# Optimization experiments

Measured on AMD Instinct MI355X. Metric: run time of the kernel, lower is better.

Reference implementation:

```python
import jax, jax.numpy as jnp
import numpy as np

SR = 48000
HARMONIC_NUM = 8          # -> 9 harmonics total
SINE_AMP = 0.1
NOISE_STD = 0.003
VOICED_THRESHOLD = 0.0
B, T, UPP = 8, 2000, 480
S = T * UPP


def setup_inputs() -> dict:
    key = jax.random.key(0)
    k_f0, k_mask, k_ri, k_noise = jax.random.split(key, 4)
    f0 = jax.random.uniform(k_f0, (B, 1, T), jnp.float32, 80.0, 500.0)
    voiced = (jax.random.uniform(k_mask, (B, 1, T)) > 0.2).astype(jnp.float32)
    f0 = f0 * voiced
    # random initial phases; harmonic 0 gets phase 0 (as in torch code)
    rand_ini = jax.random.uniform(k_ri, (B, HARMONIC_NUM + 1), jnp.float32)
    rand_ini = rand_ini.at[:, 0].set(0.0)
    noise_raw = jax.random.normal(k_noise, (B, S), jnp.float32)
    # linear mixing layer: weight = 1/(H+1), bias = 0 per nn.init in __init__
    w = jnp.full((HARMONIC_NUM + 1,), 1.0 / (HARMONIC_NUM + 1), jnp.float32)
    b = jnp.zeros((1,), jnp.float32)
    return {"f0": f0, "rand_ini": rand_ini, "noise_raw": noise_raw,
            "w": w, "b": b, "upp": UPP}


def reference(f0, rand_ini, noise_raw, w, b, upp):
    # f0: [B,1,T] Hz -> nearest-upsample to [B, S]
    f0u = jnp.repeat(f0[:, 0, :], upp, axis=1)              # [B, S]
    uv = (f0u > VOICED_THRESHOLD).astype(f0.dtype)          # [B, S]
    rad = f0u * (2.0 * np.pi / SR)
    # cumsum is linear: one cumsum, broadcast-multiply by harmonic index
    base_phase = jnp.cumsum(rad, axis=1)                    # [B, S]
    mult = jnp.arange(1, HARMONIC_NUM + 2, dtype=f0.dtype)  # [H+1]
    phase = base_phase[:, :, None] * mult + rand_ini[:, None, :] * (2.0 * np.pi)
    sines = jnp.sin(phase) * uv[:, :, None]                 # [B, S, H+1]
    har = jnp.tanh(sines @ w + b[0]) * SINE_AMP             # [B, S]
    noise = noise_raw * NOISE_STD                            # [B, S]
    return har[:, None, :], noise[:, None, :], uv[:, None, :]
```

## Files before the change

### kernel.cpp

```cpp
#include <hip/hip_runtime.h>
#include <hip/hip_bf16.h>
#include <math.h>

constexpr int   B_   = 8;
constexpr int   T_   = 2000;
constexpr int   UPP_ = 480;
constexpr int   S_   = T_ * UPP_;
constexpr int   NH   = 9;
constexpr int   SPT  = 4;
constexpr int   BLK  = 320;
constexpr int   QPR  = S_ / SPT;
constexpr int   BPR  = QPR / BLK;
constexpr float INV_SR = 1.0f / 48000.0f;

typedef float fx4 __attribute__((ext_vector_type(4)));

#if __has_builtin(__builtin_amdgcn_sinf)
__device__ __forceinline__ float sinrev(float x) { return __builtin_amdgcn_sinf(x); }
#else
__device__ __forceinline__ float sinrev(float x) { return __sinf(x * 6.2831853071795864769f); }
#endif
#if __has_builtin(__builtin_amdgcn_cosf)
__device__ __forceinline__ float cosrev(float x) { return __builtin_amdgcn_cosf(x); }
#else
__device__ __forceinline__ float cosrev(float x) { return __cosf(x * 6.2831853071795864769f); }
#endif

__device__ __forceinline__ void nt_store4(float* p, float a, float b, float c, float d) {
    fx4 v = {a, b, c, d};
    __builtin_nontemporal_store(v, (fx4*)p);
}
__device__ __forceinline__ fx4 nt_load4(const float* p) {
    return __builtin_nontemporal_load((const fx4*)p);
}

__global__ __launch_bounds__(256) void frame_scan_kernel(
    const float* __restrict__ f0,
    const float* __restrict__ rand_ini,
    const float* __restrict__ w,
    float2* __restrict__ ftab,
    float2* __restrict__ abtab)
{
    __shared__ double wsum[4];
    const int b    = blockIdx.x;
    const int j    = threadIdx.x;
    const int lane = j & 63;
    const int wid  = j >> 6;
    constexpr int CH = 8;
    const int t0 = j * CH;

    if (j < NH) {
        float ri = rand_ini[b * NH + j];
        float wv = w[j];
        abtab[b * NH + j] = make_float2(wv * cosrev(ri), wv * sinrev(ri));
    }

    float fc[CH];
    double local = 0.0;
    #pragma unroll
    for (int k = 0; k < CH; ++k) {
        int t = t0 + k;
        float v = (t < T_) ? f0[b * T_ + t] : 0.0f;
        fc[k] = v * INV_SR;
        local += (double)fc[k] * (double)UPP_;
    }

    double x = local;
    #pragma unroll
    for (int off = 1; off < 64; off <<= 1) {
        double y = __shfl_up(x, off, 64);
        if (lane >= off) x += y;
    }
    if (lane == 63) wsum[wid] = x;
    __syncthreads();

    double woff = 0.0;
    #pragma unroll
    for (int ww = 0; ww < 3; ++ww)
        if (ww < wid) woff += wsum[ww];

    double excl = (x + woff) - local;

    #pragma unroll
    for (int k = 0; k < CH; ++k) {
        int t = t0 + k;
        if (t < T_) {
            double ph = excl - floor(excl);
            ftab[b * T_ + t] = make_float2((float)ph, fc[k]);
            excl += (double)fc[k] * (double)UPP_;
        }
    }
}

__global__ __launch_bounds__(BLK) void synth_kernel(
    const float* __restrict__ noise_raw,
    const float* __restrict__ bb,
    const float2* __restrict__ ftab,
    const float2* __restrict__ abtab,
    float* __restrict__ out)
{
    const int bblk = blockIdx.x / BPR;
    const int rblk = blockIdx.x - bblk * BPR;
    const int q    = rblk * BLK + threadIdx.x;
    const int s0   = q * SPT;
    const int t    = s0 / UPP_;
    const int i0   = s0 - t * UPP_;

    float A[NH], Bc[NH];
    #pragma unroll
    for (int h = 0; h < NH; ++h) {
        float2 ab = abtab[bblk * NH + h];
        A[h]  = ab.x;
        Bc[h] = ab.y;
    }
    const float bias = bb[0];

    const float2 pf   = ftab[bblk * T_ + t];
    const float  Pred = pf.x;
    const float  fcyc = pf.y;
    const float  uvf  = (fcyc > 0.0f) ? 1.0f : 0.0f;

    const size_t row = (size_t)bblk * S_ + s0;
    const fx4 nz = nt_load4(noise_raw + row);

    float har[SPT];
    #pragma unroll
    for (int k = 0; k < SPT; ++k) {
        float base = Pred + fcyc * (float)(i0 + 1 + k);
        float f    = base - floorf(base);
        float s1   = sinrev(f);
        float c1   = cosrev(f);
        float tc   = c1 + c1;
        float sm1 = 0.0f, cm1 = 1.0f;
        float sm  = s1,   cm  = c1;
        float acc = 0.0f;
        #pragma unroll
        for (int h = 0; h < NH; ++h) {
            acc = fmaf(sm, A[h], acc);
            acc = fmaf(cm, Bc[h], acc);
            float sn = fmaf(tc, sm, -sm1);
            float cn = fmaf(tc, cm, -cm1);
            sm1 = sm; cm1 = cm; sm = sn; cm = cn;
        }
        float xx = fmaf(acc, uvf, bias);
        float e  = __expf(2.0f * xx);
        har[k]   = (e - 1.0f) / (e + 1.0f) * 0.1f;
    }

    float* harp = out;
    float* nzp  = out + (size_t)B_ * S_;
    float* uvp  = out + (size_t)2 * B_ * S_;

    nt_store4(harp + row, har[0], har[1], har[2], har[3]);
    nt_store4(nzp + row,  nz.x * 0.003f, nz.y * 0.003f, nz.z * 0.003f, nz.w * 0.003f);
    nt_store4(uvp + row,  uvf, uvf, uvf, uvf);
}

extern "C" void kernel_launch(void* const* d_in, const int* in_sizes, int n_in,
                              void* d_out, int out_size, void* d_ws, size_t ws_size,
                              hipStream_t stream) {
    const float* f0        = (const float*)d_in[0];
    const float* rand_ini  = (const float*)d_in[1];
    const float* noise_raw = (const float*)d_in[2];
    const float* w         = (const float*)d_in[3];
    const float* bb        = (const float*)d_in[4];

    float2* ftab  = (float2*)d_ws;
    float2* abtab = (float2*)((char*)d_ws + 128000);

    frame_scan_kernel<<<B_, 256, 0, stream>>>(f0, rand_ini, w, ftab, abtab);
    synth_kernel<<<B_ * BPR, BLK, 0, stream>>>(
        noise_raw, bb, ftab, abtab, (float*)d_out);
}
```

Measured before the change: 31.14 us.

## Fuse frame prefix scan into synth kernel with per-block redundant reduction

Removes the separate frame-scan kernel and its workspace tables. Each synth block now sums the f0 values of all frames before its start in a block-wide double reduction, and each thread adds the few frames between the block start and its own sample. The phase is then computed inline. This saves one kernel launch and the dependency between the two kernels, at the cost of redundant reads of f0 per block: up to 2000 values per block across 6000 blocks, plus double-precision adds and a __syncthreads.

```diff
diff --git a/kernel.cpp b/kernel.cpp
--- a/kernel.cpp
+++ b/kernel.cpp
@@ -9,9 +9,12 @@
 constexpr int   NH   = 9;
 constexpr int   SPT  = 4;
 constexpr int   BLK  = 320;
+constexpr int   SPB  = BLK * SPT;
 constexpr int   QPR  = S_ / SPT;
 constexpr int   BPR  = QPR / BLK;
+constexpr int   NWAVE = BLK / 64;
 constexpr float INV_SR = 1.0f / 48000.0f;
+constexpr double CYC_PER_F0 = (double)UPP_ / 48000.0;
 
 typedef float fx4 __attribute__((ext_vector_type(4)));
 
@@ -34,91 +37,71 @@
     return __builtin_nontemporal_load((const fx4*)p);
 }
 
-__global__ __launch_bounds__(256) void frame_scan_kernel(
+__global__ __launch_bounds__(BLK) void fused_kernel(
     const float* __restrict__ f0,
     const float* __restrict__ rand_ini,
+    const float* __restrict__ noise_raw,
     const float* __restrict__ w,
-    float2* __restrict__ ftab,
-    float2* __restrict__ abtab)
+    const float* __restrict__ bb,
+    float* __restrict__ out)
 {
-    __shared__ double wsum[4];
-    const int b    = blockIdx.x;
-    const int j    = threadIdx.x;
-    const int lane = j & 63;
-    const int wid  = j >> 6;
-    constexpr int CH = 8;
-    const int t0 = j * CH;
+    __shared__ double wpart[NWAVE];
+    __shared__ float2 ab_s[NH];
 
-    if (j < NH) {
-        float ri = rand_ini[b * NH + j];
-        float wv = w[j];
-        abtab[b * NH + j] = make_float2(wv * cosrev(ri), wv * sinrev(ri));
+    const int bblk = blockIdx.x / BPR;
+    const int rblk = blockIdx.x - bblk * BPR;
+    const int tid  = threadIdx.x;
+    const int lane = tid & 63;
+    const int wid  = tid >> 6;
+
+    const float* f0r = f0 + bblk * T_;
+
+    const int s_blk = rblk * SPB;
+    const int t_blk = s_blk / UPP_;
+
+    if (tid < NH) {
+        float ri = rand_ini[bblk * NH + tid];
+        float wv = w[tid];
+        ab_s[tid] = make_float2(wv * cosrev(ri), wv * sinrev(ri));
     }
 
-    float fc[CH];
-    double local = 0.0;
+    double lsum = 0.0;
+    for (int i = tid; i < t_blk; i += BLK)
+        lsum += (double)f0r[i];
     #pragma unroll
-    for (int k = 0; k < CH; ++k) {
-        int t = t0 + k;
-        float v = (t < T_) ? f0[b * T_ + t] : 0.0f;
-        fc[k] = v * INV_SR;
-        local += (double)fc[k] * (double)UPP_;
-    }
+    for (int off = 32; off > 0; off >>= 1)
+        lsum += __shfl_down(lsum, off, 64);
+    if (lane == 0) wpart[wid] = lsum;
+    __syncthreads();
+    double base = 0.0;
+    #pragma unroll
+    for (int ww = 0; ww < NWAVE; ++ww) base += wpart[ww];
 
-    double x = local;
-    #pragma unroll
-    for (int off = 1; off < 64; off <<= 1) {
-        double y = __shfl_up(x, off, 64);
-        if (lane >= off) x += y;
-    }
-    if (lane == 63) wsum[wid] = x;
-    __syncthreads();
+    const int q  = rblk * BLK + tid;
+    const int s0 = q * SPT;
+    const int t  = s0 / UPP_;
+    const int i0 = s0 - t * UPP_;
 
-    double woff = 0.0;
-    #pragma unroll
-    for (int ww = 0; ww < 3; ++ww)
-        if (ww < wid) woff += wsum[ww];
+    double fsum = base;
+    for (int i = t_blk; i < t; ++i)
+        fsum += (double)f0r[i];
 
-    double excl = (x + woff) - local;
+    const float fq   = f0r[t];
+    const float fcyc = fq * INV_SR;
+    const float uvf  = (fq > 0.0f) ? 1.0f : 0.0f;
 
-    #pragma unroll
-    for (int k = 0; k < CH; ++k) {
-        int t = t0 + k;
-        if (t < T_) {
-            double ph = excl - floor(excl);
-            ftab[b * T_ + t] = make_float2((float)ph, fc[k]);
-            excl += (double)fc[k] * (double)UPP_;
-        }
-    }
-}
-
-__global__ __launch_bounds__(BLK) void synth_kernel(
-    const float* __restrict__ noise_raw,
-    const float* __restrict__ bb,
-    const float2* __restrict__ ftab,
-    const float2* __restrict__ abtab,
-    float* __restrict__ out)
-{
-    const int bblk = blockIdx.x / BPR;
-    const int rblk = blockIdx.x - bblk * BPR;
-    const int q    = rblk * BLK + threadIdx.x;
-    const int s0   = q * SPT;
-    const int t    = s0 / UPP_;
-    const int i0   = s0 - t * UPP_;
+    double pc = fsum * CYC_PER_F0;
+    pc -= floor(pc);
+    const float Pred = (float)pc;
 
     float A[NH], Bc[NH];
     #pragma unroll
     for (int h = 0; h < NH; ++h) {
-        float2 ab = abtab[bblk * NH + h];
+        float2 ab = ab_s[h];
         A[h]  = ab.x;
         Bc[h] = ab.y;
     }
     const float bias = bb[0];
-
-    const float2 pf   = ftab[bblk * T_ + t];
-    const float  Pred = pf.x;
-    const float  fcyc = pf.y;
-    const float  uvf  = (fcyc > 0.0f) ? 1.0f : 0.0f;
 
     const size_t row = (size_t)bblk * S_ + s0;
     const fx4 nz = nt_load4(noise_raw + row);
@@ -126,11 +109,11 @@
     float har[SPT];
     #pragma unroll
     for (int k = 0; k < SPT; ++k) {
-        float base = Pred + fcyc * (float)(i0 + 1 + k);
-        float f    = base - floorf(base);
-        float s1   = sinrev(f);
-        float c1   = cosrev(f);
-        float tc   = c1 + c1;
+        float basef = Pred + fcyc * (float)(i0 + 1 + k);
+        float f     = basef - floorf(basef);
+        float s1    = sinrev(f);
+        float c1    = cosrev(f);
+        float tc    = c1 + c1;
         float sm1 = 0.0f, cm1 = 1.0f;
         float sm  = s1,   cm  = c1;
         float acc = 0.0f;
@@ -165,10 +148,6 @@
     const float* w         = (const float*)d_in[3];
     const float* bb        = (const float*)d_in[4];
 
-    float2* ftab  = (float2*)d_ws;
-    float2* abtab = (float2*)((char*)d_ws + 128000);
-
-    frame_scan_kernel<<<B_, 256, 0, stream>>>(f0, rand_ini, w, ftab, abtab);
-    synth_kernel<<<B_ * BPR, BLK, 0, stream>>>(
-        noise_raw, bb, ftab, abtab, (float*)d_out);
+    fused_kernel<<<B_ * BPR, BLK, 0, stream>>>(
+        f0, rand_ini, noise_raw, w, bb, (float*)d_out);
 }
```

After: 31.09 us. No clear change (-0.2%).

## Process three float4 groups per thread and use regular stores

Applied to the files above, without the earlier changes.

Each synth thread now handles three strided float4 groups, issuing all noise loads and frame-table lookups up front before computing, so more memory requests are in flight per thread and the grid is a third the size. Output stores switch from nontemporal to ordinary vector stores. This amortizes per-thread setup (loading harmonic coefficients) but raises register pressure and may reduce occupancy; dropping the nontemporal hint changes cache behavior for the streaming outputs.

```diff
diff --git a/kernel.cpp b/kernel.cpp
--- a/kernel.cpp
+++ b/kernel.cpp
@@ -7,11 +7,14 @@
 constexpr int   UPP_ = 480;
 constexpr int   S_   = T_ * UPP_;
 constexpr int   NH   = 9;
-constexpr int   SPT  = 4;
+constexpr float INV_SR = 1.0f / 48000.0f;
+
 constexpr int   BLK  = 320;
-constexpr int   QPR  = S_ / SPT;
-constexpr int   BPR  = QPR / BLK;
-constexpr float INV_SR = 1.0f / 48000.0f;
+constexpr int   J_   = 3;
+constexpr int   QPB  = BLK * J_;
+constexpr int   SPB  = QPB * 4;
+constexpr int   QPR  = S_ / 4;
+constexpr int   BPR  = QPR / QPB;
 
 typedef float fx4 __attribute__((ext_vector_type(4)));
 
@@ -26,12 +29,12 @@
 __device__ __forceinline__ float cosrev(float x) { return __cosf(x * 6.2831853071795864769f); }
 #endif
 
-__device__ __forceinline__ void nt_store4(float* p, float a, float b, float c, float d) {
-    fx4 v = {a, b, c, d};
-    __builtin_nontemporal_store(v, (fx4*)p);
-}
 __device__ __forceinline__ fx4 nt_load4(const float* p) {
     return __builtin_nontemporal_load((const fx4*)p);
+}
+__device__ __forceinline__ void st4(float* p, float a, float b, float c, float d) {
+    fx4 v = {a, b, c, d};
+    *(fx4*)p = v;
 }
 
 __global__ __launch_bounds__(256) void frame_scan_kernel(
@@ -101,10 +104,8 @@
 {
     const int bblk = blockIdx.x / BPR;
     const int rblk = blockIdx.x - bblk * BPR;
-    const int q    = rblk * BLK + threadIdx.x;
-    const int s0   = q * SPT;
-    const int t    = s0 / UPP_;
-    const int i0   = s0 - t * UPP_;
+    const int tid  = threadIdx.x;
+    const int qbase = rblk * QPB + tid;
 
     float A[NH], Bc[NH];
     #pragma unroll
@@ -115,45 +116,67 @@
     }
     const float bias = bb[0];
 
-    const float2 pf   = ftab[bblk * T_ + t];
-    const float  Pred = pf.x;
-    const float  fcyc = pf.y;
-    const float  uvf  = (fcyc > 0.0f) ? 1.0f : 0.0f;
+    const float* __restrict__ nzr = noise_raw + (size_t)bblk * S_;
+    const float2* __restrict__ ftr = ftab + bblk * T_;
 
-    const size_t row = (size_t)bblk * S_ + s0;
-    const fx4 nz = nt_load4(noise_raw + row);
+    int    s0[J_];
+    fx4    nz[J_];
+    float2 pf[J_];
 
-    float har[SPT];
     #pragma unroll
-    for (int k = 0; k < SPT; ++k) {
-        float base = Pred + fcyc * (float)(i0 + 1 + k);
-        float f    = base - floorf(base);
-        float s1   = sinrev(f);
-        float c1   = cosrev(f);
-        float tc   = c1 + c1;
-        float sm1 = 0.0f, cm1 = 1.0f;
-        float sm  = s1,   cm  = c1;
-        float acc = 0.0f;
+    for (int j = 0; j < J_; ++j) {
+        int q = qbase + j * BLK;
+        s0[j] = q * 4;
+        nz[j] = nt_load4(nzr + s0[j]);
+    }
+    #pragma unroll
+    for (int j = 0; j < J_; ++j)
+        pf[j] = ftr[s0[j] / UPP_];
+
+    float har[J_][4];
+    float uvfv[J_];
+    #pragma unroll
+    for (int j = 0; j < J_; ++j) {
+        const float Pred = pf[j].x;
+        const float fcyc = pf[j].y;
+        const float uvf  = (fcyc > 0.0f) ? 1.0f : 0.0f;
+        uvfv[j] = uvf;
+        const int  i0   = s0[j] - (s0[j] / UPP_) * UPP_;
         #pragma unroll
-        for (int h = 0; h < NH; ++h) {
-            acc = fmaf(sm, A[h], acc);
-            acc = fmaf(cm, Bc[h], acc);
-            float sn = fmaf(tc, sm, -sm1);
-            float cn = fmaf(tc, cm, -cm1);
-            sm1 = sm; cm1 = cm; sm = sn; cm = cn;
+        for (int k = 0; k < 4; ++k) {
+            float basef = Pred + fcyc * (float)(i0 + 1 + k);
+            float f     = basef - floorf(basef);
+            float s1    = sinrev(f);
+            float c1    = cosrev(f);
+            float tc    = c1 + c1;
+            float sm1 = 0.0f, cm1 = 1.0f;
+            float sm  = s1,   cm  = c1;
+            float acc = 0.0f;
+            #pragma unroll
+            for (int h = 0; h < NH; ++h) {
+                acc = fmaf(sm, A[h], acc);
+                acc = fmaf(cm, Bc[h], acc);
+                float sn = fmaf(tc, sm, -sm1);
+                float cn = fmaf(tc, cm, -cm1);
+                sm1 = sm; cm1 = cm; sm = sn; cm = cn;
+            }
+            float xx = fmaf(acc, uvf, bias);
+            float e  = __expf(2.0f * xx);
+            har[j][k] = (e - 1.0f) / (e + 1.0f) * 0.1f;
         }
-        float xx = fmaf(acc, uvf, bias);
-        float e  = __expf(2.0f * xx);
-        har[k]   = (e - 1.0f) / (e + 1.0f) * 0.1f;
     }
 
-    float* harp = out;
-    float* nzp  = out + (size_t)B_ * S_;
-    float* uvp  = out + (size_t)2 * B_ * S_;
+    float* __restrict__ harp = out + (size_t)bblk * S_;
+    float* __restrict__ nzp  = harp + (size_t)B_ * S_;
+    float* __restrict__ uvp  = harp + (size_t)2 * B_ * S_;
 
-    nt_store4(harp + row, har[0], har[1], har[2], har[3]);
-    nt_store4(nzp + row,  nz.x * 0.003f, nz.y * 0.003f, nz.z * 0.003f, nz.w * 0.003f);
-    nt_store4(uvp + row,  uvf, uvf, uvf, uvf);
+    #pragma unroll
+    for (int j = 0; j < J_; ++j) {
+        st4(harp + s0[j], har[j][0], har[j][1], har[j][2], har[j][3]);
+        st4(nzp + s0[j], nz[j].x * 0.003f, nz[j].y * 0.003f,
+                         nz[j].z * 0.003f, nz[j].w * 0.003f);
+        st4(uvp + s0[j], uvfv[j], uvfv[j], uvfv[j], uvfv[j]);
+    }
 }
 
 extern "C" void kernel_launch(void* const* d_in, const int* in_sizes, int n_in,
```

Measured after the change: 31.89 us. 1.02x slower.
